# Kernel optimization log

Measured on AMD Instinct MI355X. Metric: run time of the kernel, lower is better.

Reference implementation:

```python
import jax, jax.numpy as jnp
import numpy as np

B, T, C, NH = 8, 512, 512, 8
HD = C // NH

def _layernorm(x, g, b, eps=1e-5):
    mu = jnp.mean(x, axis=-1, keepdims=True)
    var = jnp.var(x, axis=-1, keepdims=True)
    return (x - mu) * jax.lax.rsqrt(var + eps) * g + b

def setup_inputs() -> dict:
    key = jax.random.key(0)
    ks = jax.random.split(key, 5)
    return {
        "x": jax.random.normal(ks[0], (B, T, C), jnp.float32),
        "w_attn": jax.random.normal(ks[1], (3 * C, C), jnp.float32) * (1.0 / np.sqrt(C)),
        "b_attn": jnp.zeros((3 * C,), jnp.float32),
        "w_proj": jax.random.normal(ks[2], (C, C), jnp.float32) * (1.0 / np.sqrt(C)),
        "b_proj": jnp.zeros((C,), jnp.float32),
        "q_gamma": jnp.ones((C,), jnp.float32),
        "q_beta": jnp.zeros((C,), jnp.float32),
        "k_gamma": jnp.ones((C,), jnp.float32),
        "k_beta": jnp.zeros((C,), jnp.float32),
        "rel_emb": jax.random.normal(ks[3], (T, C), jnp.float32) * 0.02,
    }

def reference(x, w_attn, b_attn, w_proj, b_proj, q_gamma, q_beta, k_gamma, k_beta, rel_emb):
    b, t, c = x.shape
    # QKV projection (torch Linear: x @ W.T + b)
    qkv = x @ w_attn.T + b_attn                       # [B,T,3C]
    q, k, v = jnp.split(qkv, 3, axis=-1)
    # per-stream LayerNorm over full embedding dim (q_ln/k_ln = LayerNorm(n_embd))
    q = _layernorm(q, q_gamma, q_beta)
    k = _layernorm(k, k_gamma, k_beta)
    # split heads -> [B,NH,T,HD]
    q = q.reshape(b, t, NH, HD).transpose(0, 2, 1, 3)
    k = k.reshape(b, t, NH, HD).transpose(0, 2, 1, 3)
    v = v.reshape(b, t, NH, HD).transpose(0, 2, 1, 3)
    # relative-position bias: gather rel_emb[|i-j|] -> [T,T,NH,HD]
    idx = jnp.abs(jnp.arange(t)[None, :] - jnp.arange(t)[:, None])  # [T,T] int
    rel = rel_emb[idx].reshape(t, t, NH, HD)
    rel_bias = jnp.einsum("bhqd,qkhd->bhqk", q, rel)  # [B,NH,T,T]
    scale = 1.0 / np.sqrt(HD)
    scores = (jnp.einsum("bhqd,bhkd->bhqk", q, k) + rel_bias) * scale
    causal = jnp.tril(jnp.ones((t, t), bool))
    scores = jnp.where(causal[None, None], scores, jnp.finfo(scores.dtype).min)
    att = jax.nn.softmax(scores, axis=-1)
    y = jnp.einsum("bhqk,bhkd->bhqd", att, v)         # [B,NH,T,HD]
    y = y.transpose(0, 2, 1, 3).reshape(b, t, c)
    return y @ w_proj.T + b_proj
```

## Files before the change

### kernel.cpp

```cpp
#include <hip/hip_runtime.h>
#include <hip/hip_bf16.h>
#include <cstddef>

#define BB 8
#define TT 512
#define CC 512
#define NHH 8
#define HDD 64

typedef __attribute__((ext_vector_type(8))) short short8;
typedef __attribute__((ext_vector_type(4))) float f32x4;

__device__ __forceinline__ unsigned short f2bf(float f) {
    unsigned u = __float_as_uint(f);
    u += 0x7FFFu + ((u >> 16) & 1u);
    return (unsigned short)(u >> 16);
}
__device__ __forceinline__ float bf2f(unsigned short h) {
    return __uint_as_float(((unsigned)h) << 16);
}

__global__ __launch_bounds__(256) void cvt_all_k(
    const float* __restrict__ x, const float* __restrict__ wa,
    const float* __restrict__ wp, const float* __restrict__ rel,
    unsigned short* __restrict__ Xb, unsigned short* __restrict__ Wqb,
    unsigned short* __restrict__ Wpb, unsigned short* __restrict__ Relb)
{
    const int bidx = blockIdx.x;
    const float* in;
    unsigned short* out;
    int base;
    if (bidx < 2048)      { in = x;   out = Xb;   base = bidx; }
    else if (bidx < 2816) { in = wa;  out = Wqb;  base = bidx - 2048; }
    else if (bidx < 3072) { in = wp;  out = Wpb;  base = bidx - 2816; }
    else                  { in = rel; out = Relb; base = bidx - 3072; }
    const int i = base * 1024 + threadIdx.x * 4;
    const float4 v = *(const float4*)(in + i);
    unsigned short tmp[4] = {f2bf(v.x), f2bf(v.y), f2bf(v.z), f2bf(v.w)};
    *(uint2*)(out + i) = *(const uint2*)tmp;
}

__global__ __launch_bounds__(256, 2) void gemm_qkv_mfma(
    const unsigned short* __restrict__ Xb, const unsigned short* __restrict__ Wb,
    const float* __restrict__ bias, float* __restrict__ qkbuf,
    unsigned short* __restrict__ VT)
{
    __shared__ __align__(16) unsigned short lds[128 * 136];

    const int tid = threadIdx.x;
    const int w = tid >> 6, lane = tid & 63;
    const int c = lane & 15, quad = lane >> 4;
    const int wm = w >> 1, wn = w & 1;
    const int bm = blockIdx.y * 128, bn = blockIdx.x * 128;

    const unsigned short* pp[8];
#pragma unroll
    for (int l = 0; l < 8; ++l) {
        const int ci = w * 8 + l;
        if (ci < 16) {
            const int m16 = ci >> 1, kk = ci & 1;
            pp[l] = Xb + (size_t)(bm + m16 * 16 + c) * 512 + kk * 32 + quad * 8;
        } else {
            const int cb = ci - 16, n16 = cb >> 1, kk = cb & 1;
            pp[l] = Wb + (size_t)(bn + n16 * 16 + c) * 512 + kk * 32 + quad * 8;
        }
    }

    f32x4 acc[4][4];
#pragma unroll
    for (int i = 0; i < 4; ++i)
#pragma unroll
        for (int j = 0; j < 4; ++j) acc[i][j] = (f32x4){0.f, 0.f, 0.f, 0.f};

    short8 pre[8];
#pragma unroll
    for (int l = 0; l < 8; ++l) pre[l] = *(const short8*)pp[l];

    for (int k0 = 0; k0 < 512; k0 += 64) {
        __syncthreads();
#pragma unroll
        for (int l = 0; l < 8; ++l)
            *(short8*)&lds[(w * 8 + l) * 512 + lane * 8] = pre[l];
        __syncthreads();
        if (k0 + 64 < 512) {
#pragma unroll
            for (int l = 0; l < 8; ++l)
                pre[l] = *(const short8*)(pp[l] + k0 + 64);
        }
#pragma unroll
        for (int kk = 0; kk < 2; ++kk) {
            short8 af[4], bfr[4];
#pragma unroll
            for (int i = 0; i < 4; ++i)
                af[i] = *(const short8*)&lds[((wm * 4 + i) * 2 + kk) * 512 + lane * 8];
#pragma unroll
            for (int j = 0; j < 4; ++j)
                bfr[j] = *(const short8*)&lds[(16 + (wn * 4 + j) * 2 + kk) * 512 + lane * 8];
#pragma unroll
            for (int i = 0; i < 4; ++i)
#pragma unroll
                for (int j = 0; j < 4; ++j)
                    acc[i][j] = __builtin_amdgcn_mfma_f32_16x16x32_bf16(
                        af[i], bfr[j], acc[i][j], 0, 0, 0);
        }
    }

    float bj[4];
#pragma unroll
    for (int j = 0; j < 4; ++j) bj[j] = bias[bn + wn * 64 + j * 16 + c];

    if (bn < 1024) {
#pragma unroll
        for (int i = 0; i < 4; ++i)
#pragma unroll
            for (int j = 0; j < 4; ++j) {
                const int n = bn + wn * 64 + j * 16 + c;
#pragma unroll
                for (int r = 0; r < 4; ++r) {
                    const int m = bm + wm * 64 + i * 16 + quad * 4 + r;
                    qkbuf[(size_t)m * 1024 + n] = acc[i][j][r] + bj[j];
                }
            }
    } else {
        __syncthreads();
#pragma unroll
        for (int i = 0; i < 4; ++i)
#pragma unroll
            for (int j = 0; j < 4; ++j) {
                const int col = wn * 64 + j * 16 + c;
                const int row0 = wm * 64 + i * 16 + quad * 4;
                unsigned short t4[4];
#pragma unroll
                for (int r = 0; r < 4; ++r) t4[r] = f2bf(acc[i][j][r] + bj[j]);
                *(uint2*)&lds[col * 136 + row0] = *(const uint2*)t4;
            }
        __syncthreads();
        const int bi = bm >> 9, tb = bm & 511;
        const int hd0 = bn - 1024;
#pragma unroll
        for (int l = 0; l < 8; ++l) {
            const int idx = l * 256 + tid;
            const int col = idx >> 4, grp = idx & 15;
            const short8 v = *(const short8*)&lds[col * 136 + grp * 8];
            const int hd = hd0 + col, h = hd >> 6, d = hd & 63;
            *(short8*)(VT + ((size_t)(bi * NHH + h) * HDD + d) * TT + tb + grp * 8) = v;
        }
    }
}

__global__ __launch_bounds__(256) void ln_k(
    const float* __restrict__ qkbuf,
    const float* __restrict__ qg, const float* __restrict__ qb,
    const float* __restrict__ kg, const float* __restrict__ kb,
    unsigned short* __restrict__ Qh, unsigned short* __restrict__ Kh)
{
    const int row = blockIdx.x;
    const int bi = row >> 9, t = row & 511;
    const float* base = qkbuf + (size_t)row * 1024;
    const int tid = threadIdx.x;
    __shared__ float red[8];
    __shared__ float stat[2];

#pragma unroll
    for (int sstr = 0; sstr < 2; ++sstr) {
        const float* p = base + sstr * 512;
        const float* gam = sstr ? kg : qg;
        const float* bet = sstr ? kb : qb;
        unsigned short* outp = sstr ? Kh : Qh;
        const float v0 = p[tid];
        const float v1 = p[tid + 256];
        float sum = v0 + v1;
        float sq = v0 * v0 + v1 * v1;
#pragma unroll
        for (int off = 32; off > 0; off >>= 1) {
            sum += __shfl_down(sum, off);
            sq += __shfl_down(sq, off);
        }
        const int lane = tid & 63, wv = tid >> 6;
        if (lane == 0) { red[wv * 2] = sum; red[wv * 2 + 1] = sq; }
        __syncthreads();
        if (tid == 0) {
            const float ts = red[0] + red[2] + red[4] + red[6];
            const float tq = red[1] + red[3] + red[5] + red[7];
            const float mu = ts * (1.f / 512.f);
            const float var = tq * (1.f / 512.f) - mu * mu;
            stat[0] = mu;
            stat[1] = rsqrtf(var + 1e-5f);
        }
        __syncthreads();
        const float mu = stat[0], rsg = stat[1];
        const float o0 = (v0 - mu) * rsg * gam[tid] + bet[tid];
        const float o1 = (v1 - mu) * rsg * gam[tid + 256] + bet[tid + 256];
        const int c0 = tid, c1 = tid + 256;
        outp[((size_t)(bi * NHH + (c0 >> 6)) * TT + t) * HDD + (c0 & 63)] = f2bf(o0);
        outp[((size_t)(bi * NHH + (c1 >> 6)) * TT + t) * HDD + (c1 & 63)] = f2bf(o1);
        __syncthreads();
    }
}

#define RD_BODY(nr_)                                                            \
    {                                                                           \
        const short8 br0 = *(const short8*)&Rels[((nr_) * 2 + 0) * 512 + lane * 8]; \
        const short8 br1 = *(const short8*)&Rels[((nr_) * 2 + 1) * 512 + lane * 8]; \
        f32x4 a2 = (f32x4){0.f, 0.f, 0.f, 0.f};                                 \
        a2 = __builtin_amdgcn_mfma_f32_16x16x32_bf16(aq0, br0, a2, 0, 0, 0);    \
        a2 = __builtin_amdgcn_mfma_f32_16x16x32_bf16(aq1, br1, a2, 0, 0, 0);    \
        const int colw = (mbase + (nr_) * 16 + c) & 127;                        \
        _Pragma("unroll")                                                       \
        for (int r = 0; r < 4; ++r)                                             \
            RDs[w][(quad * 4 + r) * 132 + colw] = f2bf(a2[r]);                  \
    }

__global__ __launch_bounds__(256, 2) void attn_k(
    const unsigned short* __restrict__ Qh, const unsigned short* __restrict__ Kh,
    const unsigned short* __restrict__ VT, const unsigned short* __restrict__ Relb,
    unsigned short* __restrict__ Yb)
{
    __shared__ __align__(16) unsigned short Qs[8 * 512];
    __shared__ __align__(16) unsigned short Ks[8 * 512];
    __shared__ __align__(16) unsigned short Vs[8 * 512];
    __shared__ __align__(16) unsigned short Rels[16 * 512];
    __shared__ __align__(16) unsigned short Ps[4][16 * 72];
    __shared__ __align__(16) unsigned short RDs[4][16 * 132];

    const int tid = threadIdx.x;
    const int w = tid >> 6;
    const int lane = tid & 63;
    const int c = lane & 15;
    const int quad = lane >> 4;
    const int qt = blockIdx.x, h = blockIdx.y, b = blockIdx.z;
    const int i0 = qt * 64;

    const unsigned short* Qbase = Qh + (size_t)(b * NHH + h) * TT * HDD;
    const unsigned short* Kbase = Kh + (size_t)(b * NHH + h) * TT * HDD;
    const unsigned short* Vbase = VT + (size_t)(b * NHH + h) * HDD * TT;
    const unsigned short* Rbase = Relb + h * HDD;

#pragma unroll
    for (int kk = 0; kk < 2; ++kk) {
        const unsigned short* gp =
            Qbase + (size_t)(i0 + w * 16 + c) * HDD + kk * 32 + quad * 8;
        *(short8*)&Qs[(w * 2 + kk) * 512 + lane * 8] = *(const short8*)gp;
    }

    f32x4 oacc[4];
    float m_i[4], l_i[4];
#pragma unroll
    for (int r = 0; r < 4; ++r) { m_i[r] = -1e30f; l_i[r] = 0.f; }
#pragma unroll
    for (int nd = 0; nd < 4; ++nd) oacc[nd] = (f32x4){0.f, 0.f, 0.f, 0.f};

    short8 aq0, aq1;

    for (int jt = 0; jt <= qt; ++jt) {
        const int j0 = jt * 64;
#pragma unroll
        for (int kk = 0; kk < 2; ++kk) {
            const unsigned short* gp =
                Kbase + (size_t)(j0 + w * 16 + c) * HDD + kk * 32 + quad * 8;
            *(short8*)&Ks[(w * 2 + kk) * 512 + lane * 8] = *(const short8*)gp;
        }
#pragma unroll
        for (int js = 0; js < 2; ++js) {
            const unsigned short* gp =
                Vbase + (size_t)(w * 16 + c) * TT + j0 + js * 32 + quad * 8;
            *(short8*)&Vs[(w * 2 + js) * 512 + lane * 8] = *(const short8*)gp;
        }
        const int mbase = i0 - j0 - 63;
        if (jt == 0) {
#pragma unroll
            for (int sb = 0; sb < 2; ++sb) {
#pragma unroll
                for (int kk = 0; kk < 2; ++kk) {
                    const int n16 = w * 2 + sb;
                    int mrow = mbase + n16 * 16 + c;
                    mrow = mrow < 0 ? 0 : (mrow > 511 ? 511 : mrow);
                    *(short8*)&Rels[(n16 * 2 + kk) * 512 + lane * 8] =
                        *(const short8*)(Rbase + (size_t)mrow * CC + kk * 32 + quad * 8);
                }
            }
        } else {
#pragma unroll
            for (int kk = 0; kk < 2; ++kk) {
                int mrow = mbase + w * 16 + c;
                mrow = mrow < 0 ? 0 : (mrow > 511 ? 511 : mrow);
                *(short8*)&Rels[(w * 2 + kk) * 512 + lane * 8] =
                    *(const short8*)(Rbase + (size_t)mrow * CC + kk * 32 + quad * 8);
            }
        }
        __syncthreads();

        if (jt == 0) {
            aq0 = *(const short8*)&Qs[(w * 2 + 0) * 512 + lane * 8];
            aq1 = *(const short8*)&Qs[(w * 2 + 1) * 512 + lane * 8];
        }

        f32x4 sAcc[4];
#pragma unroll
        for (int ns = 0; ns < 4; ++ns) {
            const short8 bk0 = *(const short8*)&Ks[(ns * 2 + 0) * 512 + lane * 8];
            const short8 bk1 = *(const short8*)&Ks[(ns * 2 + 1) * 512 + lane * 8];
            f32x4 a2 = (f32x4){0.f, 0.f, 0.f, 0.f};
            a2 = __builtin_amdgcn_mfma_f32_16x16x32_bf16(aq0, bk0, a2, 0, 0, 0);
            a2 = __builtin_amdgcn_mfma_f32_16x16x32_bf16(aq1, bk1, a2, 0, 0, 0);
            sAcc[ns] = a2;
        }
        if (jt == 0) {
#pragma unroll
            for (int nr = 0; nr < 8; ++nr) RD_BODY(nr)
        } else {
#pragma unroll
            for (int nr = 0; nr < 4; ++nr) RD_BODY(nr)
        }

        const int dbase = i0 - j0;
        float sc[4][4];
#pragma unroll
        for (int ns = 0; ns < 4; ++ns) {
#pragma unroll
            for (int r = 0; r < 4; ++r) {
                const int r16 = quad * 4 + r;
                const int jc = ns * 16 + c;
                const int dp = (dbase + w * 16 + r16 - jc) & 127;
                const float rdv = bf2f(RDs[w][r16 * 132 + dp]);
                const float v = (sAcc[ns][r] + rdv) * 0.125f;
                sc[ns][r] = (j0 + jc > i0 + w * 16 + r16) ? -1e30f : v;
            }
        }
        float alpha[4];
#pragma unroll
        for (int r = 0; r < 4; ++r) {
            float m = fmaxf(fmaxf(sc[0][r], sc[1][r]), fmaxf(sc[2][r], sc[3][r]));
#pragma unroll
            for (int off = 1; off < 16; off <<= 1) m = fmaxf(m, __shfl_xor(m, off));
            const float mn = fmaxf(m_i[r], m);
            alpha[r] = __expf(m_i[r] - mn);
            m_i[r] = mn;
        }
        float rs[4] = {0.f, 0.f, 0.f, 0.f};
#pragma unroll
        for (int ns = 0; ns < 4; ++ns) {
#pragma unroll
            for (int r = 0; r < 4; ++r) {
                const float p = __expf(sc[ns][r] - m_i[r]);
                rs[r] += p;
                Ps[w][(quad * 4 + r) * 72 + ns * 16 + c] = f2bf(p);
            }
        }
#pragma unroll
        for (int r = 0; r < 4; ++r) {
#pragma unroll
            for (int off = 1; off < 16; off <<= 1) rs[r] += __shfl_xor(rs[r], off);
            l_i[r] = l_i[r] * alpha[r] + rs[r];
        }
#pragma unroll
        for (int nd = 0; nd < 4; ++nd)
#pragma unroll
            for (int r = 0; r < 4; ++r) oacc[nd][r] *= alpha[r];

        const short8 ap0 = *(const short8*)&Ps[w][c * 72 + 0 * 32 + quad * 8];
        const short8 ap1 = *(const short8*)&Ps[w][c * 72 + 1 * 32 + quad * 8];
#pragma unroll
        for (int nd = 0; nd < 4; ++nd) {
            const short8 bv0 = *(const short8*)&Vs[(nd * 2 + 0) * 512 + lane * 8];
            const short8 bv1 = *(const short8*)&Vs[(nd * 2 + 1) * 512 + lane * 8];
            oacc[nd] = __builtin_amdgcn_mfma_f32_16x16x32_bf16(ap0, bv0, oacc[nd], 0, 0, 0);
            oacc[nd] = __builtin_amdgcn_mfma_f32_16x16x32_bf16(ap1, bv1, oacc[nd], 0, 0, 0);
        }
        __syncthreads();
    }

#pragma unroll
    for (int r = 0; r < 4; ++r) {
        const float inv = 1.f / l_i[r];
        const int trow = i0 + w * 16 + quad * 4 + r;
        unsigned short* yb = Yb + ((size_t)b * TT + trow) * CC + h * HDD;
#pragma unroll
        for (int nd = 0; nd < 4; ++nd)
            yb[nd * 16 + c] = f2bf(oacc[nd][r] * inv);
    }
}

__global__ __launch_bounds__(256, 2) void gemm_proj_mfma(
    const unsigned short* __restrict__ Yb, const unsigned short* __restrict__ Wp,
    const float* __restrict__ bias, float* __restrict__ out)
{
    __shared__ __align__(16) unsigned short lds[24 * 512];

    const int tid = threadIdx.x;
    const int w = tid >> 6, lane = tid & 63;
    const int c = lane & 15, quad = lane >> 4;
    const int wm = w >> 1, wn = w & 1;
    const int bm = blockIdx.y * 64, bn = blockIdx.x * 128;

    const unsigned short* pp[6];
#pragma unroll
    for (int l = 0; l < 6; ++l) {
        const int ci = w * 6 + l;
        if (ci < 8) {
            const int m16 = ci >> 1, kk = ci & 1;
            pp[l] = Yb + (size_t)(bm + m16 * 16 + c) * 512 + kk * 32 + quad * 8;
        } else {
            const int cb = ci - 8, n16 = cb >> 1, kk = cb & 1;
            pp[l] = Wp + (size_t)(bn + n16 * 16 + c) * 512 + kk * 32 + quad * 8;
        }
    }

    f32x4 acc[2][4];
#pragma unroll
    for (int i = 0; i < 2; ++i)
#pragma unroll
        for (int j = 0; j < 4; ++j) acc[i][j] = (f32x4){0.f, 0.f, 0.f, 0.f};

    short8 pre[6];
#pragma unroll
    for (int l = 0; l < 6; ++l) pre[l] = *(const short8*)pp[l];

    for (int k0 = 0; k0 < 512; k0 += 64) {
        __syncthreads();
#pragma unroll
        for (int l = 0; l < 6; ++l)
            *(short8*)&lds[(w * 6 + l) * 512 + lane * 8] = pre[l];
        __syncthreads();
        if (k0 + 64 < 512) {
#pragma unroll
            for (int l = 0; l < 6; ++l)
                pre[l] = *(const short8*)(pp[l] + k0 + 64);
        }
#pragma unroll
        for (int kk = 0; kk < 2; ++kk) {
            short8 af[2], bfr[4];
#pragma unroll
            for (int i = 0; i < 2; ++i)
                af[i] = *(const short8*)&lds[((wm * 2 + i) * 2 + kk) * 512 + lane * 8];
#pragma unroll
            for (int j = 0; j < 4; ++j)
                bfr[j] = *(const short8*)&lds[(8 + (wn * 4 + j) * 2 + kk) * 512 + lane * 8];
#pragma unroll
            for (int i = 0; i < 2; ++i)
#pragma unroll
                for (int j = 0; j < 4; ++j)
                    acc[i][j] = __builtin_amdgcn_mfma_f32_16x16x32_bf16(
                        af[i], bfr[j], acc[i][j], 0, 0, 0);
        }
    }

#pragma unroll
    for (int j = 0; j < 4; ++j) {
        const int n = bn + wn * 64 + j * 16 + c;
        const float bj = bias[n];
#pragma unroll
        for (int i = 0; i < 2; ++i)
#pragma unroll
            for (int r = 0; r < 4; ++r) {
                const int m = bm + wm * 32 + i * 16 + quad * 4 + r;
                out[(size_t)m * 512 + n] = acc[i][j][r] + bj;
            }
    }
}

extern "C" void kernel_launch(void* const* d_in, const int* in_sizes, int n_in,
                              void* d_out, int out_size, void* d_ws, size_t ws_size,
                              hipStream_t stream)
{
    const float* x      = (const float*)d_in[0];
    const float* w_attn = (const float*)d_in[1];
    const float* b_attn = (const float*)d_in[2];
    const float* w_proj = (const float*)d_in[3];
    const float* b_proj = (const float*)d_in[4];
    const float* q_g    = (const float*)d_in[5];
    const float* q_b    = (const float*)d_in[6];
    const float* k_g    = (const float*)d_in[7];
    const float* k_b    = (const float*)d_in[8];
    const float* rel    = (const float*)d_in[9];
    float* out = (float*)d_out;

    float* qkbuf = (float*)d_ws;
    unsigned short* Qh   = (unsigned short*)(qkbuf + (size_t)4096 * 1024);
    unsigned short* Kh   = Qh + (size_t)4096 * 512;
    unsigned short* VT   = Kh + (size_t)4096 * 512;
    unsigned short* Relb = VT + (size_t)4096 * 512;
    unsigned short* Xb   = Relb + (size_t)512 * 512;
    unsigned short* Wqb  = Xb + (size_t)4096 * 512;
    unsigned short* Wpb  = Wqb + (size_t)1536 * 512;
    unsigned short* Yb   = (unsigned short*)qkbuf;

    cvt_all_k<<<3328, 256, 0, stream>>>(x, w_attn, w_proj, rel, Xb, Wqb, Wpb, Relb);
    gemm_qkv_mfma<<<dim3(12, 32), 256, 0, stream>>>(Xb, Wqb, b_attn, qkbuf, VT);
    ln_k<<<4096, 256, 0, stream>>>(qkbuf, q_g, q_b, k_g, k_b, Qh, Kh);
    attn_k<<<dim3(8, 8, 8), 256, 0, stream>>>(Qh, Kh, VT, Relb, Yb);
    gemm_proj_mfma<<<dim3(4, 64), 256, 0, stream>>>(Yb, Wpb, b_proj, out);
}
```

Measured before the change: 149.6 us.

## Fuse fp32-to-bf16 conversion into consumers, bf16 QK buffer, warp-per-row LayerNorm

Removes the standalone conversion kernel: the QKV and projection GEMMs and the attention kernel now read fp32 x, weights and rel_emb directly and convert to bf16 while staging into LDS. The QK intermediate buffer is stored as bf16 instead of fp32, halving its write and read traffic. LayerNorm uses one wavefront per row with vectorized loads, xor-shuffle reductions and no shared memory or barriers. The attention grid is flattened and remapped so long and short causal tiles pair up for load balance. The trade-offs are double the global load bytes for the weights, which are re-read across tiles, and extra bf16 rounding applied before LayerNorm.

```diff
diff --git a/kernel.cpp b/kernel.cpp
--- a/kernel.cpp
+++ b/kernel.cpp
@@ -19,50 +19,35 @@
 __device__ __forceinline__ float bf2f(unsigned short h) {
     return __uint_as_float(((unsigned)h) << 16);
 }
-
-__global__ __launch_bounds__(256) void cvt_all_k(
-    const float* __restrict__ x, const float* __restrict__ wa,
-    const float* __restrict__ wp, const float* __restrict__ rel,
-    unsigned short* __restrict__ Xb, unsigned short* __restrict__ Wqb,
-    unsigned short* __restrict__ Wpb, unsigned short* __restrict__ Relb)
-{
-    const int bidx = blockIdx.x;
-    const float* in;
-    unsigned short* out;
-    int base;
-    if (bidx < 2048)      { in = x;   out = Xb;   base = bidx; }
-    else if (bidx < 2816) { in = wa;  out = Wqb;  base = bidx - 2048; }
-    else if (bidx < 3072) { in = wp;  out = Wpb;  base = bidx - 2816; }
-    else                  { in = rel; out = Relb; base = bidx - 3072; }
-    const int i = base * 1024 + threadIdx.x * 4;
-    const float4 v = *(const float4*)(in + i);
-    unsigned short tmp[4] = {f2bf(v.x), f2bf(v.y), f2bf(v.z), f2bf(v.w)};
-    *(uint2*)(out + i) = *(const uint2*)tmp;
+__device__ __forceinline__ short8 cvt8(float4 a, float4 b) {
+    unsigned short t[8] = {f2bf(a.x), f2bf(a.y), f2bf(a.z), f2bf(a.w),
+                           f2bf(b.x), f2bf(b.y), f2bf(b.z), f2bf(b.w)};
+    return *(const short8*)t;
 }
 
 __global__ __launch_bounds__(256, 2) void gemm_qkv_mfma(
-    const unsigned short* __restrict__ Xb, const unsigned short* __restrict__ Wb,
-    const float* __restrict__ bias, float* __restrict__ qkbuf,
+    const float* __restrict__ x, const float* __restrict__ w,
+    const float* __restrict__ bias, unsigned short* __restrict__ qkbuf,
     unsigned short* __restrict__ VT)
 {
     __shared__ __align__(16) unsigned short lds[128 * 136];
 
     const int tid = threadIdx.x;
-    const int w = tid >> 6, lane = tid & 63;
+    const int wv = tid >> 6, lane = tid & 63;
     const int c = lane & 15, quad = lane >> 4;
-    const int wm = w >> 1, wn = w & 1;
+    const int wm = wv >> 1, wn = wv & 1;
     const int bm = blockIdx.y * 128, bn = blockIdx.x * 128;
 
-    const unsigned short* pp[8];
+    const float* pp[8];
 #pragma unroll
     for (int l = 0; l < 8; ++l) {
-        const int ci = w * 8 + l;
+        const int ci = wv * 8 + l;
         if (ci < 16) {
             const int m16 = ci >> 1, kk = ci & 1;
-            pp[l] = Xb + (size_t)(bm + m16 * 16 + c) * 512 + kk * 32 + quad * 8;
+            pp[l] = x + (size_t)(bm + m16 * 16 + c) * 512 + kk * 32 + quad * 8;
         } else {
             const int cb = ci - 16, n16 = cb >> 1, kk = cb & 1;
-            pp[l] = Wb + (size_t)(bn + n16 * 16 + c) * 512 + kk * 32 + quad * 8;
+            pp[l] = w + (size_t)(bn + n16 * 16 + c) * 512 + kk * 32 + quad * 8;
         }
     }
 
@@ -72,20 +57,25 @@
 #pragma unroll
         for (int j = 0; j < 4; ++j) acc[i][j] = (f32x4){0.f, 0.f, 0.f, 0.f};
 
-    short8 pre[8];
-#pragma unroll
-    for (int l = 0; l < 8; ++l) pre[l] = *(const short8*)pp[l];
+    float4 pre0[8], pre1[8];
+#pragma unroll
+    for (int l = 0; l < 8; ++l) {
+        pre0[l] = *(const float4*)pp[l];
+        pre1[l] = *(const float4*)(pp[l] + 4);
+    }
 
     for (int k0 = 0; k0 < 512; k0 += 64) {
         __syncthreads();
 #pragma unroll
         for (int l = 0; l < 8; ++l)
-            *(short8*)&lds[(w * 8 + l) * 512 + lane * 8] = pre[l];
+            *(short8*)&lds[(wv * 8 + l) * 512 + lane * 8] = cvt8(pre0[l], pre1[l]);
         __syncthreads();
         if (k0 + 64 < 512) {
 #pragma unroll
-            for (int l = 0; l < 8; ++l)
-                pre[l] = *(const short8*)(pp[l] + k0 + 64);
+            for (int l = 0; l < 8; ++l) {
+                pre0[l] = *(const float4*)(pp[l] + k0 + 64);
+                pre1[l] = *(const float4*)(pp[l] + k0 + 68);
+            }
         }
 #pragma unroll
         for (int kk = 0; kk < 2; ++kk) {
@@ -118,7 +108,7 @@
 #pragma unroll
                 for (int r = 0; r < 4; ++r) {
                     const int m = bm + wm * 64 + i * 16 + quad * 4 + r;
-                    qkbuf[(size_t)m * 1024 + n] = acc[i][j][r] + bj[j];
+                    qkbuf[(size_t)m * 1024 + n] = f2bf(acc[i][j][r] + bj[j]);
                 }
             }
     } else {
@@ -149,52 +139,46 @@
 }
 
 __global__ __launch_bounds__(256) void ln_k(
-    const float* __restrict__ qkbuf,
+    const unsigned short* __restrict__ qkbuf,
     const float* __restrict__ qg, const float* __restrict__ qb,
     const float* __restrict__ kg, const float* __restrict__ kb,
     unsigned short* __restrict__ Qh, unsigned short* __restrict__ Kh)
 {
-    const int row = blockIdx.x;
+    const int wv = threadIdx.x >> 6, lane = threadIdx.x & 63;
+    const int row = blockIdx.x * 4 + wv;
     const int bi = row >> 9, t = row & 511;
-    const float* base = qkbuf + (size_t)row * 1024;
-    const int tid = threadIdx.x;
-    __shared__ float red[8];
-    __shared__ float stat[2];
-
-#pragma unroll
-    for (int sstr = 0; sstr < 2; ++sstr) {
-        const float* p = base + sstr * 512;
-        const float* gam = sstr ? kg : qg;
-        const float* bet = sstr ? kb : qb;
-        unsigned short* outp = sstr ? Kh : Qh;
-        const float v0 = p[tid];
-        const float v1 = p[tid + 256];
-        float sum = v0 + v1;
-        float sq = v0 * v0 + v1 * v1;
-#pragma unroll
-        for (int off = 32; off > 0; off >>= 1) {
-            sum += __shfl_down(sum, off);
-            sq += __shfl_down(sq, off);
-        }
-        const int lane = tid & 63, wv = tid >> 6;
-        if (lane == 0) { red[wv * 2] = sum; red[wv * 2 + 1] = sq; }
-        __syncthreads();
-        if (tid == 0) {
-            const float ts = red[0] + red[2] + red[4] + red[6];
-            const float tq = red[1] + red[3] + red[5] + red[7];
-            const float mu = ts * (1.f / 512.f);
-            const float var = tq * (1.f / 512.f) - mu * mu;
-            stat[0] = mu;
-            stat[1] = rsqrtf(var + 1e-5f);
-        }
-        __syncthreads();
-        const float mu = stat[0], rsg = stat[1];
-        const float o0 = (v0 - mu) * rsg * gam[tid] + bet[tid];
-        const float o1 = (v1 - mu) * rsg * gam[tid + 256] + bet[tid + 256];
-        const int c0 = tid, c1 = tid + 256;
-        outp[((size_t)(bi * NHH + (c0 >> 6)) * TT + t) * HDD + (c0 & 63)] = f2bf(o0);
-        outp[((size_t)(bi * NHH + (c1 >> 6)) * TT + t) * HDD + (c1 & 63)] = f2bf(o1);
-        __syncthreads();
+    const unsigned short* base = qkbuf + (size_t)row * 1024;
+
+#pragma unroll
+    for (int s = 0; s < 2; ++s) {
+        const short8 v8 = *(const short8*)(base + s * 512 + lane * 8);
+        float vf[8];
+#pragma unroll
+        for (int i = 0; i < 8; ++i) vf[i] = bf2f(((const unsigned short*)&v8)[i]);
+        float sum = 0.f, sq = 0.f;
+#pragma unroll
+        for (int i = 0; i < 8; ++i) { sum += vf[i]; sq += vf[i] * vf[i]; }
+#pragma unroll
+        for (int off = 1; off < 64; off <<= 1) {
+            sum += __shfl_xor(sum, off);
+            sq += __shfl_xor(sq, off);
+        }
+        const float mu = sum * (1.f / 512.f);
+        const float var = sq * (1.f / 512.f) - mu * mu;
+        const float rsg = rsqrtf(var + 1e-5f);
+        const float* gam = (s ? kg : qg) + lane * 8;
+        const float* bet = (s ? kb : qb) + lane * 8;
+        const float4 g0 = *(const float4*)gam, g1 = *(const float4*)(gam + 4);
+        const float4 b0 = *(const float4*)bet, b1 = *(const float4*)(bet + 4);
+        const float gv[8] = {g0.x, g0.y, g0.z, g0.w, g1.x, g1.y, g1.z, g1.w};
+        const float bv[8] = {b0.x, b0.y, b0.z, b0.w, b1.x, b1.y, b1.z, b1.w};
+        unsigned short o8[8];
+#pragma unroll
+        for (int i = 0; i < 8; ++i)
+            o8[i] = f2bf((vf[i] - mu) * rsg * gv[i] + bv[i]);
+        unsigned short* outp = s ? Kh : Qh;
+        *(short8*)(outp + ((size_t)(bi * NHH + (lane >> 3)) * TT + t) * HDD
+                   + (lane & 7) * 8) = *(const short8*)o8;
     }
 }
 
@@ -213,7 +197,7 @@
 
 __global__ __launch_bounds__(256, 2) void attn_k(
     const unsigned short* __restrict__ Qh, const unsigned short* __restrict__ Kh,
-    const unsigned short* __restrict__ VT, const unsigned short* __restrict__ Relb,
+    const unsigned short* __restrict__ VT, const float* __restrict__ rel,
     unsigned short* __restrict__ Yb)
 {
     __shared__ __align__(16) unsigned short Qs[8 * 512];
@@ -228,13 +212,19 @@
     const int lane = tid & 63;
     const int c = lane & 15;
     const int quad = lane >> 4;
-    const int qt = blockIdx.x, h = blockIdx.y, b = blockIdx.z;
+
+    const int bid = blockIdx.x;
+    const int half = bid >> 8, rr_ = bid & 255;
+    const int qt0 = rr_ & 7;
+    const int qt = half ? 7 - qt0 : qt0;
+    const int h = (rr_ >> 3) & 7;
+    const int b = (rr_ >> 6) + half * 4;
     const int i0 = qt * 64;
 
     const unsigned short* Qbase = Qh + (size_t)(b * NHH + h) * TT * HDD;
     const unsigned short* Kbase = Kh + (size_t)(b * NHH + h) * TT * HDD;
     const unsigned short* Vbase = VT + (size_t)(b * NHH + h) * HDD * TT;
-    const unsigned short* Rbase = Relb + h * HDD;
+    const float* Rbase = rel + h * HDD;
 
 #pragma unroll
     for (int kk = 0; kk < 2; ++kk) {
@@ -275,8 +265,9 @@
                     const int n16 = w * 2 + sb;
                     int mrow = mbase + n16 * 16 + c;
                     mrow = mrow < 0 ? 0 : (mrow > 511 ? 511 : mrow);
+                    const float* gp = Rbase + (size_t)mrow * CC + kk * 32 + quad * 8;
                     *(short8*)&Rels[(n16 * 2 + kk) * 512 + lane * 8] =
-                        *(const short8*)(Rbase + (size_t)mrow * CC + kk * 32 + quad * 8);
+                        cvt8(*(const float4*)gp, *(const float4*)(gp + 4));
                 }
             }
         } else {
@@ -284,8 +275,9 @@
             for (int kk = 0; kk < 2; ++kk) {
                 int mrow = mbase + w * 16 + c;
                 mrow = mrow < 0 ? 0 : (mrow > 511 ? 511 : mrow);
+                const float* gp = Rbase + (size_t)mrow * CC + kk * 32 + quad * 8;
                 *(short8*)&Rels[(w * 2 + kk) * 512 + lane * 8] =
-                    *(const short8*)(Rbase + (size_t)mrow * CC + kk * 32 + quad * 8);
+                    cvt8(*(const float4*)gp, *(const float4*)(gp + 4));
             }
         }
         __syncthreads();
@@ -382,7 +374,7 @@
 }
 
 __global__ __launch_bounds__(256, 2) void gemm_proj_mfma(
-    const unsigned short* __restrict__ Yb, const unsigned short* __restrict__ Wp,
+    const unsigned short* __restrict__ Yb, const float* __restrict__ Wp,
     const float* __restrict__ bias, float* __restrict__ out)
 {
     __shared__ __align__(16) unsigned short lds[24 * 512];
@@ -393,16 +385,19 @@
     const int wm = w >> 1, wn = w & 1;
     const int bm = blockIdx.y * 64, bn = blockIdx.x * 128;
 
-    const unsigned short* pp[6];
+    const unsigned short* ppA[6];
+    const float* ppB[6];
 #pragma unroll
     for (int l = 0; l < 6; ++l) {
         const int ci = w * 6 + l;
         if (ci < 8) {
             const int m16 = ci >> 1, kk = ci & 1;
-            pp[l] = Yb + (size_t)(bm + m16 * 16 + c) * 512 + kk * 32 + quad * 8;
+            ppA[l] = Yb + (size_t)(bm + m16 * 16 + c) * 512 + kk * 32 + quad * 8;
+            ppB[l] = nullptr;
         } else {
             const int cb = ci - 8, n16 = cb >> 1, kk = cb & 1;
-            pp[l] = Wp + (size_t)(bn + n16 * 16 + c) * 512 + kk * 32 + quad * 8;
+            ppA[l] = nullptr;
+            ppB[l] = Wp + (size_t)(bn + n16 * 16 + c) * 512 + kk * 32 + quad * 8;
         }
     }
 
@@ -412,20 +407,31 @@
 #pragma unroll
         for (int j = 0; j < 4; ++j) acc[i][j] = (f32x4){0.f, 0.f, 0.f, 0.f};
 
-    short8 pre[6];
-#pragma unroll
-    for (int l = 0; l < 6; ++l) pre[l] = *(const short8*)pp[l];
+    short8 preA[6];
+    float4 preB0[6], preB1[6];
+#pragma unroll
+    for (int l = 0; l < 6; ++l) {
+        if (ppA[l]) preA[l] = *(const short8*)ppA[l];
+        else { preB0[l] = *(const float4*)ppB[l]; preB1[l] = *(const float4*)(ppB[l] + 4); }
+    }
 
     for (int k0 = 0; k0 < 512; k0 += 64) {
         __syncthreads();
 #pragma unroll
-        for (int l = 0; l < 6; ++l)
-            *(short8*)&lds[(w * 6 + l) * 512 + lane * 8] = pre[l];
+        for (int l = 0; l < 6; ++l) {
+            const short8 v = ppA[l] ? preA[l] : cvt8(preB0[l], preB1[l]);
+            *(short8*)&lds[(w * 6 + l) * 512 + lane * 8] = v;
+        }
         __syncthreads();
         if (k0 + 64 < 512) {
 #pragma unroll
-            for (int l = 0; l < 6; ++l)
-                pre[l] = *(const short8*)(pp[l] + k0 + 64);
+            for (int l = 0; l < 6; ++l) {
+                if (ppA[l]) preA[l] = *(const short8*)(ppA[l] + k0 + 64);
+                else {
+                    preB0[l] = *(const float4*)(ppB[l] + k0 + 64);
+                    preB1[l] = *(const float4*)(ppB[l] + k0 + 68);
+                }
+            }
         }
 #pragma unroll
         for (int kk = 0; kk < 2; ++kk) {
@@ -475,19 +481,14 @@
     const float* rel    = (const float*)d_in[9];
     float* out = (float*)d_out;
 
-    float* qkbuf = (float*)d_ws;
-    unsigned short* Qh   = (unsigned short*)(qkbuf + (size_t)4096 * 1024);
-    unsigned short* Kh   = Qh + (size_t)4096 * 512;
-    unsigned short* VT   = Kh + (size_t)4096 * 512;
-    unsigned short* Relb = VT + (size_t)4096 * 512;
-    unsigned short* Xb   = Relb + (size_t)512 * 512;
-    unsigned short* Wqb  = Xb + (size_t)4096 * 512;
-    unsigned short* Wpb  = Wqb + (size_t)1536 * 512;
-    unsigned short* Yb   = (unsigned short*)qkbuf;
-
-    cvt_all_k<<<3328, 256, 0, stream>>>(x, w_attn, w_proj, rel, Xb, Wqb, Wpb, Relb);
-    gemm_qkv_mfma<<<dim3(12, 32), 256, 0, stream>>>(Xb, Wqb, b_attn, qkbuf, VT);
-    ln_k<<<4096, 256, 0, stream>>>(qkbuf, q_g, q_b, k_g, k_b, Qh, Kh);
-    attn_k<<<dim3(8, 8, 8), 256, 0, stream>>>(Qh, Kh, VT, Relb, Yb);
-    gemm_proj_mfma<<<dim3(4, 64), 256, 0, stream>>>(Yb, Wpb, b_proj, out);
-}
+    unsigned short* qkbuf = (unsigned short*)d_ws;
+    unsigned short* Qh = qkbuf + (size_t)4096 * 1024;
+    unsigned short* Kh = Qh + (size_t)4096 * 512;
+    unsigned short* VT = Kh + (size_t)4096 * 512;
+    unsigned short* Yb = qkbuf;
+
+    gemm_qkv_mfma<<<dim3(12, 32), 256, 0, stream>>>(x, w_attn, b_attn, qkbuf, VT);
+    ln_k<<<1024, 256, 0, stream>>>(qkbuf, q_g, q_b, k_g, k_b, Qh, Kh);
+    attn_k<<<512, 256, 0, stream>>>(Qh, Kh, VT, rel, Yb);
+    gemm_proj_mfma<<<dim3(4, 64), 256, 0, stream>>>(Yb, w_proj, b_proj, out);
+}
```

Result: slower. 162.5 us (+8.6%).

## Store QK intermediate as bf16, warp-per-row LayerNorm, remap attention blocks for balance

Applied to the files above, without the earlier changes.

The QKV GEMM now writes the Q/K pre-norm buffer in bf16 instead of fp32, halving that intermediate's write and read traffic. LayerNorm is rewritten so each wavefront handles one row with vectorized 8-element loads and xor-shuffle reductions, with no shared memory or block barriers. The attention grid is flattened to 1D with a block-index permutation that pairs causal query tiles (qt and 7-qt) to balance work across CUs. Rounding pre-LN values to bf16 adds precision loss before the normalization statistics are computed.

```diff
diff --git a/kernel.cpp b/kernel.cpp
--- a/kernel.cpp
+++ b/kernel.cpp
@@ -42,7 +42,7 @@
 
 __global__ __launch_bounds__(256, 2) void gemm_qkv_mfma(
     const unsigned short* __restrict__ Xb, const unsigned short* __restrict__ Wb,
-    const float* __restrict__ bias, float* __restrict__ qkbuf,
+    const float* __restrict__ bias, unsigned short* __restrict__ qkbuf,
     unsigned short* __restrict__ VT)
 {
     __shared__ __align__(16) unsigned short lds[128 * 136];
@@ -118,7 +118,7 @@
 #pragma unroll
                 for (int r = 0; r < 4; ++r) {
                     const int m = bm + wm * 64 + i * 16 + quad * 4 + r;
-                    qkbuf[(size_t)m * 1024 + n] = acc[i][j][r] + bj[j];
+                    qkbuf[(size_t)m * 1024 + n] = f2bf(acc[i][j][r] + bj[j]);
                 }
             }
     } else {
@@ -149,52 +149,46 @@
 }
 
 __global__ __launch_bounds__(256) void ln_k(
-    const float* __restrict__ qkbuf,
+    const unsigned short* __restrict__ qkbuf,
     const float* __restrict__ qg, const float* __restrict__ qb,
     const float* __restrict__ kg, const float* __restrict__ kb,
     unsigned short* __restrict__ Qh, unsigned short* __restrict__ Kh)
 {
-    const int row = blockIdx.x;
+    const int wv = threadIdx.x >> 6, lane = threadIdx.x & 63;
+    const int row = blockIdx.x * 4 + wv;
     const int bi = row >> 9, t = row & 511;
-    const float* base = qkbuf + (size_t)row * 1024;
-    const int tid = threadIdx.x;
-    __shared__ float red[8];
-    __shared__ float stat[2];
-
-#pragma unroll
-    for (int sstr = 0; sstr < 2; ++sstr) {
-        const float* p = base + sstr * 512;
-        const float* gam = sstr ? kg : qg;
-        const float* bet = sstr ? kb : qb;
-        unsigned short* outp = sstr ? Kh : Qh;
-        const float v0 = p[tid];
-        const float v1 = p[tid + 256];
-        float sum = v0 + v1;
-        float sq = v0 * v0 + v1 * v1;
-#pragma unroll
-        for (int off = 32; off > 0; off >>= 1) {
-            sum += __shfl_down(sum, off);
-            sq += __shfl_down(sq, off);
-        }
-        const int lane = tid & 63, wv = tid >> 6;
-        if (lane == 0) { red[wv * 2] = sum; red[wv * 2 + 1] = sq; }
-        __syncthreads();
-        if (tid == 0) {
-            const float ts = red[0] + red[2] + red[4] + red[6];
-            const float tq = red[1] + red[3] + red[5] + red[7];
-            const float mu = ts * (1.f / 512.f);
-            const float var = tq * (1.f / 512.f) - mu * mu;
-            stat[0] = mu;
-            stat[1] = rsqrtf(var + 1e-5f);
-        }
-        __syncthreads();
-        const float mu = stat[0], rsg = stat[1];
-        const float o0 = (v0 - mu) * rsg * gam[tid] + bet[tid];
-        const float o1 = (v1 - mu) * rsg * gam[tid + 256] + bet[tid + 256];
-        const int c0 = tid, c1 = tid + 256;
-        outp[((size_t)(bi * NHH + (c0 >> 6)) * TT + t) * HDD + (c0 & 63)] = f2bf(o0);
-        outp[((size_t)(bi * NHH + (c1 >> 6)) * TT + t) * HDD + (c1 & 63)] = f2bf(o1);
-        __syncthreads();
+    const unsigned short* base = qkbuf + (size_t)row * 1024;
+
+#pragma unroll
+    for (int s = 0; s < 2; ++s) {
+        const short8 v8 = *(const short8*)(base + s * 512 + lane * 8);
+        float vf[8];
+#pragma unroll
+        for (int i = 0; i < 8; ++i) vf[i] = bf2f(((const unsigned short*)&v8)[i]);
+        float sum = 0.f, sq = 0.f;
+#pragma unroll
+        for (int i = 0; i < 8; ++i) { sum += vf[i]; sq += vf[i] * vf[i]; }
+#pragma unroll
+        for (int off = 1; off < 64; off <<= 1) {
+            sum += __shfl_xor(sum, off);
+            sq += __shfl_xor(sq, off);
+        }
+        const float mu = sum * (1.f / 512.f);
+        const float var = sq * (1.f / 512.f) - mu * mu;
+        const float rsg = rsqrtf(var + 1e-5f);
+        const float* gam = (s ? kg : qg) + lane * 8;
+        const float* bet = (s ? kb : qb) + lane * 8;
+        const float4 g0 = *(const float4*)gam, g1 = *(const float4*)(gam + 4);
+        const float4 b0 = *(const float4*)bet, b1 = *(const float4*)(bet + 4);
+        const float gv[8] = {g0.x, g0.y, g0.z, g0.w, g1.x, g1.y, g1.z, g1.w};
+        const float bv[8] = {b0.x, b0.y, b0.z, b0.w, b1.x, b1.y, b1.z, b1.w};
+        unsigned short o8[8];
+#pragma unroll
+        for (int i = 0; i < 8; ++i)
+            o8[i] = f2bf((vf[i] - mu) * rsg * gv[i] + bv[i]);
+        unsigned short* outp = s ? Kh : Qh;
+        *(short8*)(outp + ((size_t)(bi * NHH + (lane >> 3)) * TT + t) * HDD
+                   + (lane & 7) * 8) = *(const short8*)o8;
     }
 }
 
@@ -228,7 +222,14 @@
     const int lane = tid & 63;
     const int c = lane & 15;
     const int quad = lane >> 4;
-    const int qt = blockIdx.x, h = blockIdx.y, b = blockIdx.z;
+
+    const int bid = blockIdx.x;
+    const int bit0 = bid & 1, bit8 = (bid >> 8) & 1;
+    const int s_ = bit0 ^ bit8;
+    const int q0 = (bid >> 1) & 7;
+    const int qt = s_ ? 7 - q0 : q0;
+    const int h = (bid >> 4) & 7;
+    const int b = ((bid >> 7) & 1) | (bit8 << 1) | (bit0 << 2);
     const int i0 = qt * 64;
 
     const unsigned short* Qbase = Qh + (size_t)(b * NHH + h) * TT * HDD;
@@ -475,19 +476,19 @@
     const float* rel    = (const float*)d_in[9];
     float* out = (float*)d_out;
 
-    float* qkbuf = (float*)d_ws;
-    unsigned short* Qh   = (unsigned short*)(qkbuf + (size_t)4096 * 1024);
+    unsigned short* qkbuf = (unsigned short*)d_ws;
+    unsigned short* Qh   = qkbuf + (size_t)4096 * 1024;
     unsigned short* Kh   = Qh + (size_t)4096 * 512;
     unsigned short* VT   = Kh + (size_t)4096 * 512;
     unsigned short* Relb = VT + (size_t)4096 * 512;
     unsigned short* Xb   = Relb + (size_t)512 * 512;
     unsigned short* Wqb  = Xb + (size_t)4096 * 512;
     unsigned short* Wpb  = Wqb + (size_t)1536 * 512;
-    unsigned short* Yb   = (unsigned short*)qkbuf;
+    unsigned short* Yb   = qkbuf;
 
     cvt_all_k<<<3328, 256, 0, stream>>>(x, w_attn, w_proj, rel, Xb, Wqb, Wpb, Relb);
     gemm_qkv_mfma<<<dim3(12, 32), 256, 0, stream>>>(Xb, Wqb, b_attn, qkbuf, VT);
-    ln_k<<<4096, 256, 0, stream>>>(qkbuf, q_g, q_b, k_g, k_b, Qh, Kh);
-    attn_k<<<dim3(8, 8, 8), 256, 0, stream>>>(Qh, Kh, VT, Relb, Yb);
+    ln_k<<<1024, 256, 0, stream>>>(qkbuf, q_g, q_b, k_g, k_b, Qh, Kh);
+    attn_k<<<512, 256, 0, stream>>>(Qh, Kh, VT, Relb, Yb);
     gemm_proj_mfma<<<dim3(4, 64), 256, 0, stream>>>(Yb, Wpb, b_proj, out);
 }
```

Measured after the change: 141.6 us. 1.06x faster.
